# Kernel tuning notes

Measured on AMD Instinct MI355X. Metric: run time of the kernel, lower is better.

## Reference

```python
import jax, jax.numpy as jnp
import numpy as np

N, E, IN_F, OUT_F, HEADS, SLOPE = 20000, 160000, 512, 256, 6, 0.2


def _gat_conv(x, src, dst, W, att_src, att_dst, bias, out_ch):
    # PyG GATConv, concat=False (mean over heads), self-loops already in src/dst
    n = x.shape[0]
    xp = (x @ W).reshape(n, HEADS, out_ch)              # [N,H,C]
    a_src = (xp * att_src).sum(-1)                      # [N,H]
    a_dst = (xp * att_dst).sum(-1)                      # [N,H]
    alpha = jax.nn.leaky_relu(a_src[src] + a_dst[dst], SLOPE)  # [Et,H]
    amax = jax.ops.segment_max(alpha, dst, num_segments=n)
    amax = jnp.where(jnp.isfinite(amax), amax, 0.0)
    ex = jnp.exp(alpha - amax[dst])
    denom = jax.ops.segment_sum(ex, dst, num_segments=n)
    coef = ex / (denom[dst] + 1e-16)                    # edge softmax per dst node
    msg = xp[src] * coef[:, :, None]                    # [Et,H,C]
    out = jax.ops.segment_sum(msg, dst, num_segments=n) # [N,H,C]
    return out.mean(axis=1) + bias


def setup_inputs() -> dict:
    key = jax.random.key(0)
    ks = jax.random.split(key, 10)
    s = 0.05
    return {
        "data": jax.random.uniform(ks[0], (N, IN_F), dtype=jnp.float32),
        "edge_idx": jax.random.randint(ks[1], (2, E), 0, N, dtype=jnp.int64),
        "W_coord": jax.random.normal(ks[2], (IN_F, HEADS * 2), dtype=jnp.float32) * s,
        "att_src_coord": jax.random.normal(ks[3], (HEADS, 2), dtype=jnp.float32) * s,
        "att_dst_coord": jax.random.normal(ks[4], (HEADS, 2), dtype=jnp.float32) * s,
        "b_coord": jnp.zeros((2,), dtype=jnp.float32),
        "W_feat": jax.random.normal(ks[5], (IN_F, HEADS * OUT_F), dtype=jnp.float32) * s,
        "att_src_feat": jax.random.normal(ks[6], (HEADS, OUT_F), dtype=jnp.float32) * s,
        "att_dst_feat": jax.random.normal(ks[7], (HEADS, OUT_F), dtype=jnp.float32) * s,
        "b_feat": jnp.zeros((OUT_F,), dtype=jnp.float32),
    }


def reference(data, edge_idx, W_coord, att_src_coord, att_dst_coord, b_coord,
              W_feat, att_src_feat, att_dst_feat, b_feat):
    n = data.shape[0]
    loop = jnp.arange(n, dtype=edge_idx.dtype)
    src = jnp.concatenate([edge_idx[0], loop])  # PyG adds self-loops by default
    dst = jnp.concatenate([edge_idx[1], loop])

    coord = _gat_conv(data, src, dst, W_coord, att_src_coord, att_dst_coord, b_coord, 2)
    feat = _gat_conv(data, src, dst, W_feat, att_src_feat, att_dst_feat, b_feat, OUT_F)
    feat = jax.nn.selu(feat)

    # find_boundary + fix_boundary
    coord = coord.at[:, 0].set(jnp.where(data[:, 0] == 1, 1.0, coord[:, 0]))
    coord = coord.at[:, 0].set(jnp.where(data[:, 0] == 0, 0.0, coord[:, 0]))
    coord = coord.at[:, 1].set(jnp.where(data[:, 1] == 0, 0.0, coord[:, 1]))
    coord = coord.at[:, 1].set(jnp.where(data[:, 1] == 1, 1.0, coord[:, 1]))
    return (coord, feat)
```

## Files before the change

kernel.cpp:

```cpp
#include <hip/hip_runtime.h>
#include <hip/hip_bf16.h>
#include <math.h>

#define NF_IN 512
#define NF_OUT 256
#define HEADS 6
#define NCOLS (HEADS * NF_OUT)
#define K2 (HEADS * NF_IN)
#define SLOPE 0.2f

typedef __attribute__((ext_vector_type(8))) short short8;
typedef __attribute__((ext_vector_type(4))) float f32x4;

__device__ __forceinline__ float bf2f(unsigned short u) {
  unsigned int x = ((unsigned int)u) << 16;
  return __uint_as_float(x);
}
__device__ __forceinline__ unsigned short f2bf(float f) {
  unsigned int x = __float_as_uint(f);
  unsigned int lsb = (x >> 16) & 1u;
  x += 0x7fffu + lsb;
  return (unsigned short)(x >> 16);
}

__device__ __forceinline__ void gload_lds16(const void* g, void* l) {
  __builtin_amdgcn_global_load_lds(
      (const __attribute__((address_space(1))) void*)g,
      (__attribute__((address_space(3))) void*)l, 16, 0, 0);
}

__global__ void zero_kernel(int* __restrict__ p, int n) {
  int i = blockIdx.x * blockDim.x + threadIdx.x;
  if (i < n) p[i] = 0;
}

__global__ __launch_bounds__(256) void watt_kernel(
    const float* __restrict__ Wf, const float* __restrict__ Wc,
    const float* __restrict__ att_s, const float* __restrict__ att_d,
    float* __restrict__ wcomb) {
  int wid = threadIdx.x >> 6, lane = threadIdx.x & 63;
  int k = blockIdx.x * 4 + wid;
  if (lane < 12) wcomb[lane * NF_IN + k] = Wc[k * 12 + lane];
#pragma unroll
  for (int h = 0; h < HEADS; ++h) {
    float4 w = *(const float4*)(Wf + (size_t)k * NCOLS + h * NF_OUT + lane * 4);
    float4 as = *(const float4*)(att_s + h * NF_OUT + lane * 4);
    float4 ad = *(const float4*)(att_d + h * NF_OUT + lane * 4);
    float s = w.x * as.x + w.y * as.y + w.z * as.z + w.w * as.w;
    float d = w.x * ad.x + w.y * ad.y + w.z * ad.z + w.w * ad.w;
#pragma unroll
    for (int off = 32; off; off >>= 1) {
      s += __shfl_xor(s, off, 64);
      d += __shfl_xor(d, off, 64);
    }
    if (lane == 0) {
      wcomb[(12 + h) * NF_IN + k] = s;
      wcomb[(18 + h) * NF_IN + k] = d;
    }
  }
}

__global__ __launch_bounds__(256) void prep_data_kernel(
    const float* __restrict__ data, const float* __restrict__ wcomb,
    const float* __restrict__ att_src_c, const float* __restrict__ att_dst_c,
    unsigned short* __restrict__ data_bf, float* __restrict__ xp,
    float* __restrict__ asc, float* __restrict__ adc,
    float* __restrict__ asf, float* __restrict__ adf, int n_nodes) {
  __shared__ __align__(16) unsigned short Wb[24 * NF_IN];
  int t = threadIdx.x;
#pragma unroll
  for (int i = 0; i < 3; ++i) {
    int c = i * 256 + t;
    const float* src = wcomb + c * 16;
    float4 a = *(const float4*)(src);
    float4 b = *(const float4*)(src + 4);
    float4 cc = *(const float4*)(src + 8);
    float4 d = *(const float4*)(src + 12);
    ushort4 u0, u1, u2, u3;
    u0.x = f2bf(a.x); u0.y = f2bf(a.y); u0.z = f2bf(a.z); u0.w = f2bf(a.w);
    u1.x = f2bf(b.x); u1.y = f2bf(b.y); u1.z = f2bf(b.z); u1.w = f2bf(b.w);
    u2.x = f2bf(cc.x); u2.y = f2bf(cc.y); u2.z = f2bf(cc.z); u2.w = f2bf(cc.w);
    u3.x = f2bf(d.x); u3.y = f2bf(d.y); u3.z = f2bf(d.z); u3.w = f2bf(d.w);
    *(ushort4*)(Wb + c * 16) = u0;
    *(ushort4*)(Wb + c * 16 + 4) = u1;
    *(ushort4*)(Wb + c * 16 + 8) = u2;
    *(ushort4*)(Wb + c * 16 + 12) = u3;
  }
  __syncthreads();
  int lane = t & 63;
  int gw = blockIdx.x * 4 + (t >> 6);
  int nw = gridDim.x * 4;
  for (int n = gw; n < n_nodes; n += nw) {
    const float* row = data + (size_t)n * NF_IN + lane * 8;
    float x[8];
    *(float4*)(x) = *(const float4*)(row);
    *(float4*)(x + 4) = *(const float4*)(row + 4);
    ushort4 b0, b1;
    b0.x = f2bf(x[0]); b0.y = f2bf(x[1]); b0.z = f2bf(x[2]); b0.w = f2bf(x[3]);
    b1.x = f2bf(x[4]); b1.y = f2bf(x[5]); b1.z = f2bf(x[6]); b1.w = f2bf(x[7]);
    unsigned short* db = data_bf + (size_t)n * NF_IN + lane * 8;
    *(ushort4*)(db) = b0;
    *(ushort4*)(db + 4) = b1;
    float acc[24];
#pragma unroll
    for (int o = 0; o < 24; ++o) {
      short8 w = *(const short8*)(Wb + o * NF_IN + lane * 8);
      float a = 0.f;
#pragma unroll
      for (int j = 0; j < 8; ++j) a += x[j] * bf2f((unsigned short)w[j]);
      acc[o] = a;
    }
#pragma unroll
    for (int o = 0; o < 24; ++o) {
#pragma unroll
      for (int off = 32; off; off >>= 1) acc[o] += __shfl_xor(acc[o], off, 64);
    }
    if (lane == 0) {
      float* xr = xp + (size_t)n * 12;
#pragma unroll
      for (int o = 0; o < 12; ++o) xr[o] = acc[o];
#pragma unroll
      for (int h = 0; h < HEADS; ++h) {
        asc[n * HEADS + h] = acc[2 * h] * att_src_c[2 * h] + acc[2 * h + 1] * att_src_c[2 * h + 1];
        adc[n * HEADS + h] = acc[2 * h] * att_dst_c[2 * h] + acc[2 * h + 1] * att_dst_c[2 * h + 1];
        asf[n * HEADS + h] = acc[12 + h];
        adf[n * HEADS + h] = acc[18 + h];
      }
    }
  }
}

__global__ __launch_bounds__(256) void transpose_w2_kernel(
    const float* __restrict__ W, unsigned short* __restrict__ Wt2) {
  __shared__ float tileS[32][33];
  int col0 = blockIdx.x * 32;
  int k0 = blockIdx.y * 32;
  int t = threadIdx.x;
  int tr = t >> 5;
  int tc = t & 31;
#pragma unroll
  for (int j = 0; j < 4; ++j)
    tileS[tr * 4 + j][tc] = W[(size_t)(k0 + tr * 4 + j) * NCOLS + col0 + tc];
  __syncthreads();
  int head = col0 >> 8;
  int cbase = col0 & 255;
#pragma unroll
  for (int j = 0; j < 4; ++j)
    Wt2[(size_t)(cbase + tr * 4 + j) * K2 + head * NF_IN + k0 + tc] =
        f2bf(tileS[tc][tr * 4 + j]);
}

__global__ void count_edges_kernel(const int* __restrict__ ei, int E, int Et,
                                   int* __restrict__ counts) {
  int e = blockIdx.x * blockDim.x + threadIdx.x;
  if (e >= Et) return;
  int d = (e < E) ? ei[E + e] : (e - E);
  atomicAdd(&counts[d], 1);
}

__global__ __launch_bounds__(1024) void scan_kernel(const int* __restrict__ counts,
                                                    int* __restrict__ indptr, int n) {
  __shared__ int wsum[16];
  const int CH = (n + 1023) >> 10;
  int t = threadIdx.x, lane = t & 63, w = t >> 6;
  int base = t * CH;
  int run = 0;
  for (int i = 0; i < CH; ++i) {
    int idx = base + i;
    run += (idx < n) ? counts[idx] : 0;
  }
  int tot = run;
#pragma unroll
  for (int off = 1; off < 64; off <<= 1) {
    int x = __shfl_up(tot, off, 64);
    if (lane >= off) tot += x;
  }
  if (lane == 63) wsum[w] = tot;
  __syncthreads();
  if (t == 0) {
    int s = 0;
#pragma unroll
    for (int i = 0; i < 16; ++i) { int x = wsum[i]; wsum[i] = s; s += x; }
  }
  __syncthreads();
  int run2 = wsum[w] + (tot - run);
  if (t == 0) indptr[0] = 0;
  for (int i = 0; i < CH; ++i) {
    int idx = base + i;
    if (idx < n) {
      run2 += counts[idx];
      indptr[idx + 1] = run2;
    }
  }
}

__global__ void scatter_kernel(const int* __restrict__ ei, int E, int Et,
                               const int* __restrict__ indptr, int* __restrict__ fill,
                               int* __restrict__ csr_src) {
  int e = blockIdx.x * blockDim.x + threadIdx.x;
  if (e >= Et) return;
  int s, d;
  if (e < E) { s = ei[e]; d = ei[E + e]; } else { s = d = e - E; }
  int pos = indptr[d] + atomicAdd(&fill[d], 1);
  csr_src[pos] = s;
}

__global__ __launch_bounds__(256) void softmax_coord_kernel(
    const float* __restrict__ asf, const float* __restrict__ adf,
    const float* __restrict__ asc, const float* __restrict__ adc,
    const int* __restrict__ indptr, const int* __restrict__ csr_src,
    const float* __restrict__ xpc, const float* __restrict__ b_coord,
    const float* __restrict__ data, float* __restrict__ coef_f,
    float* __restrict__ inv_f, float* __restrict__ out_coord, int n_nodes) {
  int gid = blockIdx.x * blockDim.x + threadIdx.x;
  int n = gid >> 3;
  int h = gid & 7;
  bool act = (n < n_nodes) && (h < HEADS);
  int e0 = 0, e1 = 0;
  float adF = 0.f, adC = 0.f;
  if (act) {
    e0 = indptr[n];
    e1 = indptr[n + 1];
    adF = adf[n * HEADS + h];
    adC = adc[n * HEADS + h];
  }
  float sF = 0.f, sC = 0.f, c0 = 0.f, c1 = 0.f;
  for (int p = e0; p < e1; ++p) {
    int s = csr_src[p];
    float vF = asf[s * HEADS + h] + adF;
    float vC = asc[s * HEADS + h] + adC;
    vF = (vF >= 0.f) ? vF : SLOPE * vF;
    vC = (vC >= 0.f) ? vC : SLOPE * vC;
    float eF = __expf(vF);
    float eC = __expf(vC);
    coef_f[(size_t)p * HEADS + h] = eF;
    sF += eF;
    sC += eC;
    c0 += eC * xpc[(size_t)s * 12 + 2 * h];
    c1 += eC * xpc[(size_t)s * 12 + 2 * h + 1];
  }
  if (act) inv_f[n * HEADS + h] = 1.f / (sF + 1e-16f);
  float iC = (1.f / (sC + 1e-16f)) * (1.f / HEADS);
  c0 *= iC;
  c1 *= iC;
#pragma unroll
  for (int off = 1; off < 8; off <<= 1) {
    c0 += __shfl_xor(c0, off, 8);
    c1 += __shfl_xor(c1, off, 8);
  }
  if (h == 0 && n < n_nodes) {
    c0 += b_coord[0];
    c1 += b_coord[1];
    float d0 = data[(size_t)n * NF_IN + 0];
    float d1 = data[(size_t)n * NF_IN + 1];
    if (d0 == 1.f) c0 = 1.f;
    if (d0 == 0.f) c0 = 0.f;
    if (d1 == 0.f) c1 = 0.f;
    if (d1 == 1.f) c1 = 1.f;
    out_coord[(size_t)n * 2 + 0] = c0;
    out_coord[(size_t)n * 2 + 1] = c1;
  }
}

__global__ __launch_bounds__(256) void agg_data_kernel(
    const unsigned short* __restrict__ xb, const float* __restrict__ coef,
    const float* __restrict__ invf, const int* __restrict__ indptr,
    const int* __restrict__ csr_src, unsigned short* __restrict__ AGG, int n_nodes) {
  int lane = threadIdx.x & 63;
  int gw = blockIdx.x * 4 + (threadIdx.x >> 6);
  int nw = gridDim.x * 4;
  const unsigned short* xbl = xb + lane * 8;

  for (int n = gw; n < n_nodes; n += nw) {
    int e0 = indptr[n], e1 = indptr[n + 1];
    float inv[HEADS];
#pragma unroll
    for (int h = 0; h < HEADS; ++h) inv[h] = invf[n * HEADS + h];
    float acc[HEADS][8];
#pragma unroll
    for (int h = 0; h < HEADS; ++h)
#pragma unroll
      for (int i = 0; i < 8; ++i) acc[h][i] = 0.f;

    int p = e0;
    for (; p + 4 <= e1; p += 4) {
      int s0 = csr_src[p], s1 = csr_src[p + 1], s2 = csr_src[p + 2], s3 = csr_src[p + 3];
      short8 v0 = *(const short8*)(xbl + (size_t)s0 * NF_IN);
      short8 v1 = *(const short8*)(xbl + (size_t)s1 * NF_IN);
      short8 v2 = *(const short8*)(xbl + (size_t)s2 * NF_IN);
      short8 v3 = *(const short8*)(xbl + (size_t)s3 * NF_IN);
      float cf[4][HEADS];
#pragma unroll
      for (int e = 0; e < 4; ++e)
#pragma unroll
        for (int h = 0; h < HEADS; ++h) cf[e][h] = coef[(size_t)(p + e) * HEADS + h];
      float f0[8], f1[8], f2[8], f3[8];
#pragma unroll
      for (int i = 0; i < 8; ++i) {
        f0[i] = bf2f((unsigned short)v0[i]);
        f1[i] = bf2f((unsigned short)v1[i]);
        f2[i] = bf2f((unsigned short)v2[i]);
        f3[i] = bf2f((unsigned short)v3[i]);
      }
#pragma unroll
      for (int h = 0; h < HEADS; ++h)
#pragma unroll
        for (int i = 0; i < 8; ++i)
          acc[h][i] += cf[0][h] * f0[i] + cf[1][h] * f1[i] +
                       cf[2][h] * f2[i] + cf[3][h] * f3[i];
    }
    for (; p < e1; ++p) {
      int s0 = csr_src[p];
      short8 v0 = *(const short8*)(xbl + (size_t)s0 * NF_IN);
      float f0[8];
#pragma unroll
      for (int i = 0; i < 8; ++i) f0[i] = bf2f((unsigned short)v0[i]);
#pragma unroll
      for (int h = 0; h < HEADS; ++h) {
        float c = coef[(size_t)p * HEADS + h];
#pragma unroll
        for (int i = 0; i < 8; ++i) acc[h][i] += c * f0[i];
      }
    }
    unsigned short* og = AGG + (size_t)n * K2 + lane * 8;
#pragma unroll
    for (int h = 0; h < HEADS; ++h) {
      short8 w;
#pragma unroll
      for (int i = 0; i < 8; ++i) w[i] = (short)f2bf(acc[h][i] * inv[h]);
      *(short8*)(og + h * NF_IN) = w;
    }
  }
}

#define G2M 64
#define G2N 64
#define G2K 64
__global__ __launch_bounds__(256) void gemm2_kernel(
    const unsigned short* __restrict__ A, const unsigned short* __restrict__ Bt,
    const float* __restrict__ bias, float* __restrict__ outF, int M, int npan) {
  __shared__ __align__(16) unsigned short sA[G2M * G2K];
  __shared__ __align__(16) unsigned short sB[G2N * G2K];
  int b = blockIdx.x;
  int nwg = npan * 4;
  int q = nwg >> 3, r = nwg & 7;
  int xcd = b & 7, slot = b >> 3;
  int base = xcd * q + (xcd < r ? xcd : r);
  int nid = base + slot;
  int row0 = (nid >> 2) * G2M;
  int col0 = (nid & 3) * G2N;

  const int tid = threadIdx.x;
  const int wid = tid >> 6;
  const int lane = tid & 63;
  const int wr = (wid >> 1) * 32;
  const int wc = (wid & 1) * 32;

  f32x4 acc[2][2] = {};

  const int kseg = lane & 7;
  const int srow0 = (tid >> 3);
  const int swz0 = (kseg ^ (srow0 & 7)) * 8;
  const int swz1 = (kseg ^ ((srow0 + 32) & 7)) * 8;
  int ar0 = row0 + srow0; if (ar0 >= M) ar0 = M - 1;
  int ar1 = row0 + srow0 + 32; if (ar1 >= M) ar1 = M - 1;
  const unsigned short* gA0 = A + (size_t)ar0 * K2 + swz0;
  const unsigned short* gA1 = A + (size_t)ar1 * K2 + swz1;
  const unsigned short* gB0 = Bt + (size_t)(col0 + srow0) * K2 + swz0;
  const unsigned short* gB1 = Bt + (size_t)(col0 + srow0 + 32) * K2 + swz1;
  unsigned short* lA = sA + wid * 512;
  unsigned short* lB = sB + wid * 512;

  const int fr = lane & 15;
  const int g0 = lane >> 4;

  for (int k0 = 0; k0 < K2; k0 += G2K) {
    gload_lds16(gA0 + k0, lA);
    gload_lds16(gA1 + k0, lA + 2048);
    gload_lds16(gB0 + k0, lB);
    gload_lds16(gB1 + k0, lB + 2048);
    __syncthreads();
#pragma unroll
    for (int s = 0; s < 2; ++s) {
      short8 af[2], bfr[2];
#pragma unroll
      for (int m = 0; m < 2; ++m) {
        int rr = wr + m * 16 + fr;
        int gp = ((s * 4 + g0) ^ (rr & 7)) * 8;
        af[m] = *(const short8*)(sA + rr * G2K + gp);
      }
#pragma unroll
      for (int nn = 0; nn < 2; ++nn) {
        int rr = wc + nn * 16 + fr;
        int gp = ((s * 4 + g0) ^ (rr & 7)) * 8;
        bfr[nn] = *(const short8*)(sB + rr * G2K + gp);
      }
#pragma unroll
      for (int m = 0; m < 2; ++m)
#pragma unroll
        for (int nn = 0; nn < 2; ++nn)
          acc[m][nn] = __builtin_amdgcn_mfma_f32_16x16x32_bf16(af[m], bfr[nn],
                                                               acc[m][nn], 0, 0, 0);
    }
    __syncthreads();
  }

  const float selu_scale = 1.0507009873554805f;
  const float selu_alpha = 1.6732632423543772f;
  const int dcol = lane & 15;
  const int g4 = (lane >> 4) * 4;
#pragma unroll
  for (int m = 0; m < 2; ++m) {
#pragma unroll
    for (int i = 0; i < 4; ++i) {
      int rr = row0 + wr + m * 16 + g4 + i;
      if (rr < M) {
#pragma unroll
        for (int nn = 0; nn < 2; ++nn) {
          int c = col0 + wc + nn * 16 + dcol;
          float v = acc[m][nn][i] * (1.f / HEADS) + bias[c];
          v = (v > 0.f) ? selu_scale * v : selu_scale * selu_alpha * expm1f(v);
          outF[(size_t)rr * NF_OUT + c] = v;
        }
      }
    }
  }
}

extern "C" void kernel_launch(void* const* d_in, const int* in_sizes, int n_in,
                              void* d_out, int out_size, void* d_ws, size_t ws_size,
                              hipStream_t stream) {
  const float* data = (const float*)d_in[0];
  const int* ei = (const int*)d_in[1];
  const float* W_coord = (const float*)d_in[2];
  const float* att_src_coord = (const float*)d_in[3];
  const float* att_dst_coord = (const float*)d_in[4];
  const float* b_coord = (const float*)d_in[5];
  const float* W_feat = (const float*)d_in[6];
  const float* att_src_feat = (const float*)d_in[7];
  const float* att_dst_feat = (const float*)d_in[8];
  const float* b_feat = (const float*)d_in[9];
  float* out = (float*)d_out;

  const int n = in_sizes[0] / NF_IN;
  const int E = in_sizes[1] / 2;
  const int Et = E + n;

  char* ws = (char*)d_ws;
  size_t o = 0;
  unsigned short* AGG = (unsigned short*)(ws + o); o += (size_t)n * K2 * 2;
  unsigned short* data_bf = (unsigned short*)(ws + o); o += (size_t)n * NF_IN * 2;
  unsigned short* w2t = (unsigned short*)(ws + o); o += (size_t)NF_OUT * K2 * 2;
  float* wcomb = (float*)(ws + o); o += (size_t)NF_IN * 24 * 4;
  float* xp_coord = (float*)(ws + o); o += (size_t)n * 12 * 4;
  float* asf = (float*)(ws + o); o += (size_t)n * HEADS * 4;
  float* adf = (float*)(ws + o); o += (size_t)n * HEADS * 4;
  float* asc = (float*)(ws + o); o += (size_t)n * HEADS * 4;
  float* adc = (float*)(ws + o); o += (size_t)n * HEADS * 4;
  float* inv_f = (float*)(ws + o); o += (size_t)n * HEADS * 4;
  int* counts = (int*)(ws + o); o += (size_t)n * 4;
  int* fill = (int*)(ws + o); o += (size_t)n * 4;
  int* indptr = (int*)(ws + o); o += ((size_t)n + 32) * 4;
  int* csr_src = (int*)(ws + o); o += (size_t)Et * 4;
  float* coef_f = (float*)(ws + o); o += (size_t)Et * HEADS * 4;
  if (o > ws_size) return;

  zero_kernel<<<(2 * n + 255) / 256, 256, 0, stream>>>(counts, 2 * n);
  watt_kernel<<<128, 256, 0, stream>>>(W_feat, W_coord, att_src_feat, att_dst_feat, wcomb);
  prep_data_kernel<<<512, 256, 0, stream>>>(data, wcomb, att_src_coord,
                                            att_dst_coord, data_bf, xp_coord,
                                            asc, adc, asf, adf, n);
  {
    dim3 grid(NCOLS / 32, NF_IN / 32);
    transpose_w2_kernel<<<grid, 256, 0, stream>>>(W_feat, w2t);
  }
  count_edges_kernel<<<(Et + 255) / 256, 256, 0, stream>>>(ei, E, Et, counts);
  scan_kernel<<<1, 1024, 0, stream>>>(counts, indptr, n);
  scatter_kernel<<<(Et + 255) / 256, 256, 0, stream>>>(ei, E, Et, indptr, fill, csr_src);
  {
    int nb = (n * 8 + 255) / 256;
    softmax_coord_kernel<<<nb, 256, 0, stream>>>(asf, adf, asc, adc, indptr, csr_src,
                                                 xp_coord, b_coord, data, coef_f, inv_f,
                                                 out, n);
  }
  agg_data_kernel<<<2048, 256, 0, stream>>>(data_bf, coef_f, inv_f, indptr, csr_src,
                                            AGG, n);
  {
    int npan = (n + G2M - 1) / G2M;
    gemm2_kernel<<<npan * 4, 256, 0, stream>>>(AGG, w2t, b_feat, out + (size_t)n * 2,
                                               n, npan);
  }
}
```

Before: 212.5 us.

## Split aggregation heads across two waves and merge weight-prep kernels

The aggregation kernel now assigns each node to two wavefronts, each handling three of the six heads. This halves the per-wave accumulator registers, which should raise occupancy and parallelism, at the cost of each source row being gathered twice. The weight projection and the weight transpose kernels are merged into one launch, and the zero kernel is replaced by hipMemsetAsync, cutting launch count.

```diff
diff --git a/kernel.cpp b/kernel.cpp
--- a/kernel.cpp
+++ b/kernel.cpp
@@ -29,34 +29,50 @@
       (__attribute__((address_space(3))) void*)l, 16, 0, 0);
 }
 
-__global__ void zero_kernel(int* __restrict__ p, int n) {
-  int i = blockIdx.x * blockDim.x + threadIdx.x;
-  if (i < n) p[i] = 0;
-}
-
-__global__ __launch_bounds__(256) void watt_kernel(
+__global__ __launch_bounds__(256) void wprep_kernel(
     const float* __restrict__ Wf, const float* __restrict__ Wc,
     const float* __restrict__ att_s, const float* __restrict__ att_d,
-    float* __restrict__ wcomb) {
-  int wid = threadIdx.x >> 6, lane = threadIdx.x & 63;
-  int k = blockIdx.x * 4 + wid;
-  if (lane < 12) wcomb[lane * NF_IN + k] = Wc[k * 12 + lane];
-#pragma unroll
-  for (int h = 0; h < HEADS; ++h) {
-    float4 w = *(const float4*)(Wf + (size_t)k * NCOLS + h * NF_OUT + lane * 4);
-    float4 as = *(const float4*)(att_s + h * NF_OUT + lane * 4);
-    float4 ad = *(const float4*)(att_d + h * NF_OUT + lane * 4);
-    float s = w.x * as.x + w.y * as.y + w.z * as.z + w.w * as.w;
-    float d = w.x * ad.x + w.y * ad.y + w.z * ad.z + w.w * ad.w;
-#pragma unroll
-    for (int off = 32; off; off >>= 1) {
-      s += __shfl_xor(s, off, 64);
-      d += __shfl_xor(d, off, 64);
-    }
-    if (lane == 0) {
-      wcomb[(12 + h) * NF_IN + k] = s;
-      wcomb[(18 + h) * NF_IN + k] = d;
-    }
+    float* __restrict__ wcomb, unsigned short* __restrict__ Wt2) {
+  int bid = blockIdx.x;
+  if (bid < 128) {
+    int wid = threadIdx.x >> 6, lane = threadIdx.x & 63;
+    int k = bid * 4 + wid;
+    if (lane < 12) wcomb[lane * NF_IN + k] = Wc[k * 12 + lane];
+#pragma unroll
+    for (int h = 0; h < HEADS; ++h) {
+      float4 w = *(const float4*)(Wf + (size_t)k * NCOLS + h * NF_OUT + lane * 4);
+      float4 as = *(const float4*)(att_s + h * NF_OUT + lane * 4);
+      float4 ad = *(const float4*)(att_d + h * NF_OUT + lane * 4);
+      float s = w.x * as.x + w.y * as.y + w.z * as.z + w.w * as.w;
+      float d = w.x * ad.x + w.y * ad.y + w.z * ad.z + w.w * ad.w;
+#pragma unroll
+      for (int off = 32; off; off >>= 1) {
+        s += __shfl_xor(s, off, 64);
+        d += __shfl_xor(d, off, 64);
+      }
+      if (lane == 0) {
+        wcomb[(12 + h) * NF_IN + k] = s;
+        wcomb[(18 + h) * NF_IN + k] = d;
+      }
+    }
+  } else {
+    __shared__ float tileS[32][33];
+    int b2 = bid - 128;
+    int col0 = (b2 % 48) * 32;
+    int k0 = (b2 / 48) * 32;
+    int t = threadIdx.x;
+    int tr = t >> 5;
+    int tc = t & 31;
+#pragma unroll
+    for (int j = 0; j < 4; ++j)
+      tileS[tr * 4 + j][tc] = Wf[(size_t)(k0 + tr * 4 + j) * NCOLS + col0 + tc];
+    __syncthreads();
+    int head = col0 >> 8;
+    int cbase = col0 & 255;
+#pragma unroll
+    for (int j = 0; j < 4; ++j)
+      Wt2[(size_t)(cbase + tr * 4 + j) * K2 + head * NF_IN + k0 + tc] =
+          f2bf(tileS[tc][tr * 4 + j]);
   }
 }
 
@@ -128,26 +144,6 @@
       }
     }
   }
-}
-
-__global__ __launch_bounds__(256) void transpose_w2_kernel(
-    const float* __restrict__ W, unsigned short* __restrict__ Wt2) {
-  __shared__ float tileS[32][33];
-  int col0 = blockIdx.x * 32;
-  int k0 = blockIdx.y * 32;
-  int t = threadIdx.x;
-  int tr = t >> 5;
-  int tc = t & 31;
-#pragma unroll
-  for (int j = 0; j < 4; ++j)
-    tileS[tr * 4 + j][tc] = W[(size_t)(k0 + tr * 4 + j) * NCOLS + col0 + tc];
-  __syncthreads();
-  int head = col0 >> 8;
-  int cbase = col0 & 255;
-#pragma unroll
-  for (int j = 0; j < 4; ++j)
-    Wt2[(size_t)(cbase + tr * 4 + j) * K2 + head * NF_IN + k0 + tc] =
-        f2bf(tileS[tc][tr * 4 + j]);
 }
 
 __global__ void count_edges_kernel(const int* __restrict__ ei, int E, int Et,
@@ -268,19 +264,21 @@
     const int* __restrict__ csr_src, unsigned short* __restrict__ AGG, int n_nodes) {
   int lane = threadIdx.x & 63;
   int gw = blockIdx.x * 4 + (threadIdx.x >> 6);
-  int nw = gridDim.x * 4;
+  int half = gw & 1;
+  int h0 = half * 3;
+  int nstep = (gridDim.x * 4) >> 1;
   const unsigned short* xbl = xb + lane * 8;
 
-  for (int n = gw; n < n_nodes; n += nw) {
+  for (int n = gw >> 1; n < n_nodes; n += nstep) {
     int e0 = indptr[n], e1 = indptr[n + 1];
-    float inv[HEADS];
-#pragma unroll
-    for (int h = 0; h < HEADS; ++h) inv[h] = invf[n * HEADS + h];
-    float acc[HEADS][8];
-#pragma unroll
-    for (int h = 0; h < HEADS; ++h)
-#pragma unroll
-      for (int i = 0; i < 8; ++i) acc[h][i] = 0.f;
+    float inv[3];
+#pragma unroll
+    for (int j = 0; j < 3; ++j) inv[j] = invf[n * HEADS + h0 + j];
+    float acc[3][8];
+#pragma unroll
+    for (int j = 0; j < 3; ++j)
+#pragma unroll
+      for (int i = 0; i < 8; ++i) acc[j][i] = 0.f;
 
     int p = e0;
     for (; p + 4 <= e1; p += 4) {
@@ -289,46 +287,57 @@
       short8 v1 = *(const short8*)(xbl + (size_t)s1 * NF_IN);
       short8 v2 = *(const short8*)(xbl + (size_t)s2 * NF_IN);
       short8 v3 = *(const short8*)(xbl + (size_t)s3 * NF_IN);
-      float cf[4][HEADS];
+      float cf[4][3];
 #pragma unroll
       for (int e = 0; e < 4; ++e)
 #pragma unroll
-        for (int h = 0; h < HEADS; ++h) cf[e][h] = coef[(size_t)(p + e) * HEADS + h];
-      float f0[8], f1[8], f2[8], f3[8];
-#pragma unroll
-      for (int i = 0; i < 8; ++i) {
-        f0[i] = bf2f((unsigned short)v0[i]);
-        f1[i] = bf2f((unsigned short)v1[i]);
-        f2[i] = bf2f((unsigned short)v2[i]);
-        f3[i] = bf2f((unsigned short)v3[i]);
-      }
-#pragma unroll
-      for (int h = 0; h < HEADS; ++h)
-#pragma unroll
-        for (int i = 0; i < 8; ++i)
-          acc[h][i] += cf[0][h] * f0[i] + cf[1][h] * f1[i] +
-                       cf[2][h] * f2[i] + cf[3][h] * f3[i];
+        for (int j = 0; j < 3; ++j) cf[e][j] = coef[(size_t)(p + e) * HEADS + h0 + j];
+      float f[8];
+#pragma unroll
+      for (int i = 0; i < 8; ++i) f[i] = bf2f((unsigned short)v0[i]);
+#pragma unroll
+      for (int j = 0; j < 3; ++j)
+#pragma unroll
+        for (int i = 0; i < 8; ++i) acc[j][i] += cf[0][j] * f[i];
+#pragma unroll
+      for (int i = 0; i < 8; ++i) f[i] = bf2f((unsigned short)v1[i]);
+#pragma unroll
+      for (int j = 0; j < 3; ++j)
+#pragma unroll
+        for (int i = 0; i < 8; ++i) acc[j][i] += cf[1][j] * f[i];
+#pragma unroll
+      for (int i = 0; i < 8; ++i) f[i] = bf2f((unsigned short)v2[i]);
+#pragma unroll
+      for (int j = 0; j < 3; ++j)
+#pragma unroll
+        for (int i = 0; i < 8; ++i) acc[j][i] += cf[2][j] * f[i];
+#pragma unroll
+      for (int i = 0; i < 8; ++i) f[i] = bf2f((unsigned short)v3[i]);
+#pragma unroll
+      for (int j = 0; j < 3; ++j)
+#pragma unroll
+        for (int i = 0; i < 8; ++i) acc[j][i] += cf[3][j] * f[i];
     }
     for (; p < e1; ++p) {
       int s0 = csr_src[p];
       short8 v0 = *(const short8*)(xbl + (size_t)s0 * NF_IN);
-      float f0[8];
-#pragma unroll
-      for (int i = 0; i < 8; ++i) f0[i] = bf2f((unsigned short)v0[i]);
-#pragma unroll
-      for (int h = 0; h < HEADS; ++h) {
-        float c = coef[(size_t)p * HEADS + h];
-#pragma unroll
-        for (int i = 0; i < 8; ++i) acc[h][i] += c * f0[i];
-      }
-    }
-    unsigned short* og = AGG + (size_t)n * K2 + lane * 8;
-#pragma unroll
-    for (int h = 0; h < HEADS; ++h) {
+      float f[8];
+#pragma unroll
+      for (int i = 0; i < 8; ++i) f[i] = bf2f((unsigned short)v0[i]);
+#pragma unroll
+      for (int j = 0; j < 3; ++j) {
+        float c = coef[(size_t)p * HEADS + h0 + j];
+#pragma unroll
+        for (int i = 0; i < 8; ++i) acc[j][i] += c * f[i];
+      }
+    }
+    unsigned short* og = AGG + (size_t)n * K2 + (size_t)h0 * NF_IN + lane * 8;
+#pragma unroll
+    for (int j = 0; j < 3; ++j) {
       short8 w;
 #pragma unroll
-      for (int i = 0; i < 8; ++i) w[i] = (short)f2bf(acc[h][i] * inv[h]);
-      *(short8*)(og + h * NF_IN) = w;
+      for (int i = 0; i < 8; ++i) w[i] = (short)f2bf(acc[j][i] * inv[j]);
+      *(short8*)(og + j * NF_IN) = w;
     }
   }
 }
@@ -465,15 +474,12 @@
   float* coef_f = (float*)(ws + o); o += (size_t)Et * HEADS * 4;
   if (o > ws_size) return;
 
-  zero_kernel<<<(2 * n + 255) / 256, 256, 0, stream>>>(counts, 2 * n);
-  watt_kernel<<<128, 256, 0, stream>>>(W_feat, W_coord, att_src_feat, att_dst_feat, wcomb);
+  hipMemsetAsync(counts, 0, (size_t)2 * n * 4, stream);
+  wprep_kernel<<<128 + (NCOLS / 32) * (NF_IN / 32), 256, 0, stream>>>(
+      W_feat, W_coord, att_src_feat, att_dst_feat, wcomb, w2t);
   prep_data_kernel<<<512, 256, 0, stream>>>(data, wcomb, att_src_coord,
                                             att_dst_coord, data_bf, xp_coord,
                                             asc, adc, asf, adf, n);
-  {
-    dim3 grid(NCOLS / 32, NF_IN / 32);
-    transpose_w2_kernel<<<grid, 256, 0, stream>>>(W_feat, w2t);
-  }
   count_edges_kernel<<<(Et + 255) / 256, 256, 0, stream>>>(ei, E, Et, counts);
   scan_kernel<<<1, 1024, 0, stream>>>(counts, indptr, n);
   scatter_kernel<<<(Et + 255) / 256, 256, 0, stream>>>(ei, E, Et, indptr, fill, csr_src);
```

Result: no change. 211.8 us (-0.3%).
